# Performance work log

Hardware: AMD Instinct MI355X
Metric: run time of the kernel (lower is better)

The kernel has to match this reference:

```python
import jax, jax.numpy as jnp
import numpy as np

B, T, DIM = 1, 1024, 1024
H = 8
QLR, KVLR = 768, 512
DNOPE, DROPE, DV = 128, 64, 128
DK = DNOPE + DROPE  # 192
EPS = 1e-5


def _rms(x, w):
    return x * jax.lax.rsqrt(jnp.mean(x * x, axis=-1, keepdims=True) + EPS) * w


def _l2norm(x):
    return x * jax.lax.rsqrt(jnp.sum(x * x, axis=-1, keepdims=True) + 1e-6)


def setup_inputs() -> dict:
    key = jax.random.key(0)
    ks = jax.random.split(key, 12)
    std = 0.02
    rnd = lambda k, shape: (jax.random.normal(k, shape, dtype=jnp.float32) * std)
    return {
        'x': jax.random.normal(ks[0], (B, T, DIM), dtype=jnp.float32),
        'cos': jax.random.normal(ks[1], (T, DROPE), dtype=jnp.float32),
        'sin': jax.random.normal(ks[2], (T, DROPE), dtype=jnp.float32),
        'wq_a': rnd(ks[3], (DIM, QLR)),
        'q_norm_w': jnp.ones((QLR,), dtype=jnp.float32),
        'wq_b': rnd(ks[4], (QLR, H * DK)),
        'wkv_a': rnd(ks[5], (DIM, KVLR + DROPE)),
        'kv_norm_w': jnp.ones((KVLR,), dtype=jnp.float32),
        'wkv_b': rnd(ks[6], (KVLR, H * (DNOPE + DV))),
        'wg_w': rnd(ks[7], (DIM, H * DK)),
        'wg_b': jnp.zeros((H * DK,), dtype=jnp.float32),
        'wb': rnd(ks[8], (DIM, H)),
        'wo': rnd(ks[9], (H * DV, DIM)),
    }


def _kda(q, k, v, g, beta):
    # q,k: [B,T,H,DK]; v: [B,T,H,DV]; g: [B,T,H,DK] (log-decay); beta: [B,T,H]
    q = _l2norm(q) * (DK ** -0.5)
    k = _l2norm(k)
    # time-major for scan
    qs = jnp.moveaxis(q, 1, 0)
    ks_ = jnp.moveaxis(k, 1, 0)
    vs = jnp.moveaxis(v, 1, 0)
    gs = jnp.moveaxis(g, 1, 0)
    bs = jnp.moveaxis(beta, 1, 0)

    def step(S, inp):
        q_t, k_t, v_t, g_t, b_t = inp  # [B,H,DK],[B,H,DK],[B,H,DV],[B,H,DK],[B,H]
        S = S * jnp.exp(g_t)[..., None]                       # per-key-dim decay
        u_t = b_t[..., None] * (v_t - jnp.einsum('bhk,bhkv->bhv', k_t, S))
        S = S + k_t[..., None] * u_t[..., None, :]            # rank-1 delta update
        o_t = jnp.einsum('bhk,bhkv->bhv', q_t, S)
        return S, o_t

    S0 = jnp.zeros((B, H, DK, DV), dtype=q.dtype)
    _, o = jax.lax.scan(step, S0, (qs, ks_, vs, gs, bs))
    return jnp.moveaxis(o, 0, 1)  # [B,T,H,DV]


def reference(x, cos, sin, wq_a, q_norm_w, wq_b, wkv_a, kv_norm_w, wkv_b, wg_w, wg_b, wb, wo):
    # cos/sin are accepted but unused, matching the original forward body.
    q = (_rms(x @ wq_a, q_norm_w) @ wq_b).reshape(B, T, H, DK)
    kv_all = x @ wkv_a
    kv_c, k_pe = kv_all[..., :KVLR], kv_all[..., KVLR:]       # [B,T,KVLR],[B,T,DROPE]
    kv = (_rms(kv_c, kv_norm_w) @ wkv_b).reshape(B, T, H, DNOPE + DV)
    k_nope, v = kv[..., :DNOPE], kv[..., DNOPE:]
    k = jnp.concatenate(
        [k_nope, jnp.broadcast_to(k_pe[:, :, None, :], (B, T, H, DROPE))], axis=-1)
    g = jax.nn.log_sigmoid(x @ wg_w + wg_b).reshape(B, T, H, DK)
    beta = jax.nn.sigmoid(x @ wb).reshape(B, T, H)
    o = _kda(q, k, v, g, beta)
    o = jnp.nan_to_num(o, nan=0.0, posinf=10000.0, neginf=-10000.0)
    return o.reshape(B, T, H * DV) @ wo
```

## Files before the change

kernel.cpp:

```cpp
#include <hip/hip_runtime.h>
#include <hip/hip_bf16.h>
#include <math.h>

#define TT 1024
#define DIM 1024
#define HH 8
#define QLR 768
#define KVLR 512
#define DNOPE 128
#define DROPE 64
#define DV 128
#define DK 192
#define HDK (HH*DK)
#define HKV (HH*(DNOPE+DV))

#define OY   0
#define OQ   3072
#define OC   6144
#define OPL  9984
#define OU   10240
#define OLAM 12288
#define PABLK 12480

typedef __attribute__((ext_vector_type(8))) short short8;
typedef __attribute__((ext_vector_type(4))) float f32x4;

__device__ __forceinline__ unsigned short f2bf_rn(float f) {
    unsigned u = __float_as_uint(f);
    unsigned lsb = (u >> 16) & 1u;
    u += 0x7fffu + lsb;
    return (unsigned short)(u >> 16);
}
__device__ __forceinline__ float bf2f(unsigned short h) {
    return __uint_as_float(((unsigned)h) << 16);
}

__global__ __launch_bounds__(256) void wconv(
    const float* __restrict__ W0, unsigned short* __restrict__ H0,
    unsigned short* __restrict__ L0, int K0, int N0, int T0,
    const float* __restrict__ W1, unsigned short* __restrict__ H1,
    unsigned short* __restrict__ L1, int K1, int N1, int T1,
    const float* __restrict__ W2, unsigned short* __restrict__ H2,
    unsigned short* __restrict__ L2, int K2, int N2, int T2)
{
    __shared__ float Ls[64][65];
    int bx = blockIdx.x;
    const float* W; unsigned short* H; unsigned short* L; int K, N;
    if (bx < T0)           { W = W0; H = H0; L = L0; K = K0; N = N0; }
    else if (bx < T0 + T1) { bx -= T0; W = W1; H = H1; L = L1; K = K1; N = N1; }
    else                   { bx -= T0 + T1; W = W2; H = H2; L = L2; K = K2; N = N2; }

    const int NT = N >> 6;
    const int kt = bx / NT, nt = bx - kt * NT;
    const int k0 = kt * 64, n0 = nt * 64;
    const int tid = threadIdx.x;
    const int r = tid >> 2, c = (tid & 3) * 16;

#pragma unroll
    for (int i = 0; i < 4; i++)
        *(float4*)&Ls[r][c + i * 4] =
            *(const float4*)&W[(size_t)(k0 + r) * N + n0 + c + i * 4];
    __syncthreads();

    const int nr = tid >> 2, kc = (tid & 3) * 16;
    unsigned short hb[16], lb[16];
#pragma unroll
    for (int j = 0; j < 16; j++) {
        float v = Ls[kc + j][nr];
        unsigned short h = f2bf_rn(v);
        hb[j] = h;
        lb[j] = f2bf_rn(v - bf2f(h));
    }
    size_t ob = (size_t)(n0 + nr) * K + k0 + kc;
    *(float4*)&H[ob]     = ((float4*)hb)[0];
    *(float4*)&H[ob + 8] = ((float4*)hb)[1];
    *(float4*)&L[ob]     = ((float4*)lb)[0];
    *(float4*)&L[ob + 8] = ((float4*)lb)[1];
}

__global__ __launch_bounds__(256) void aconv(
    const float* __restrict__ A, unsigned short* __restrict__ H,
    unsigned short* __restrict__ L)
{
    int i = (blockIdx.x * 256 + threadIdx.x) * 8;
    float4 v0 = *(const float4*)&A[i];
    float4 v1 = *(const float4*)&A[i + 4];
    float vv[8] = {v0.x, v0.y, v0.z, v0.w, v1.x, v1.y, v1.z, v1.w};
    unsigned short hb[8], lb[8];
#pragma unroll
    for (int j = 0; j < 8; j++) {
        unsigned short h = f2bf_rn(vv[j]);
        hb[j] = h;
        lb[j] = f2bf_rn(vv[j] - bf2f(h));
    }
    *(float4*)&H[i] = *(float4*)hb;
    *(float4*)&L[i] = *(float4*)lb;
}

__global__ __launch_bounds__(128) void gemm_bt(
    const unsigned short* __restrict__ Ah0, const unsigned short* __restrict__ Al0,
    const unsigned short* __restrict__ Bh0, const unsigned short* __restrict__ Bl0,
    float* __restrict__ C0, int K0, int N0, int T0,
    const unsigned short* __restrict__ Ah1, const unsigned short* __restrict__ Al1,
    const unsigned short* __restrict__ Bh1, const unsigned short* __restrict__ Bl1,
    float* __restrict__ C1, int K1, int N1, int T1,
    const unsigned short* __restrict__ Ah2, const unsigned short* __restrict__ Al2,
    const unsigned short* __restrict__ Bh2, const unsigned short* __restrict__ Bl2,
    float* __restrict__ C2, int K2, int N2, int T2)
{
    __shared__ unsigned short Ahs[64 * 40], Als[64 * 40];
    __shared__ unsigned short Bhs[64 * 40], Bls[64 * 40];

    int bx = blockIdx.x;
    const unsigned short *Ah, *Al, *Bh, *Bl; float* C; int K, N;
    if (bx < T0) {
        Ah = Ah0; Al = Al0; Bh = Bh0; Bl = Bl0; C = C0; K = K0; N = N0;
    } else if (bx < T0 + T1) {
        bx -= T0; Ah = Ah1; Al = Al1; Bh = Bh1; Bl = Bl1; C = C1; K = K1; N = N1;
    } else {
        bx -= T0 + T1; Ah = Ah2; Al = Al2; Bh = Bh2; Bl = Bl2; C = C2; K = K2; N = N2;
    }

    const int tid = threadIdx.x;
    const int w = tid >> 6, l = tid & 63;
    const int q = l >> 4, m16 = l & 15;
    const int bm = blockIdx.y * 64, bn = bx * 64;

    const int c0i = tid * 2, c1i = tid * 2 + 1;
    const int r0 = c0i >> 2, o0 = (c0i & 3) * 8;
    const int r1 = c1i >> 2, o1 = (c1i & 3) * 8;
    const unsigned short* pAh0 = Ah + (size_t)(bm + r0) * K + o0;
    const unsigned short* pAh1 = Ah + (size_t)(bm + r1) * K + o1;
    const unsigned short* pAl0 = Al + (size_t)(bm + r0) * K + o0;
    const unsigned short* pAl1 = Al + (size_t)(bm + r1) * K + o1;
    const unsigned short* pBh0 = Bh + (size_t)(bn + r0) * K + o0;
    const unsigned short* pBh1 = Bh + (size_t)(bn + r1) * K + o1;
    const unsigned short* pBl0 = Bl + (size_t)(bn + r0) * K + o0;
    const unsigned short* pBl1 = Bl + (size_t)(bn + r1) * K + o1;

    f32x4 acc[2][4];
#pragma unroll
    for (int i = 0; i < 2; i++)
#pragma unroll
        for (int j = 0; j < 4; j++)
            acc[i][j] = (f32x4){0.f, 0.f, 0.f, 0.f};

    float4 vAh0 = *(const float4*)pAh0, vAh1 = *(const float4*)pAh1;
    float4 vAl0 = *(const float4*)pAl0, vAl1 = *(const float4*)pAl1;
    float4 vBh0 = *(const float4*)pBh0, vBh1 = *(const float4*)pBh1;
    float4 vBl0 = *(const float4*)pBl0, vBl1 = *(const float4*)pBl1;

    for (int k0 = 0;; k0 += 32) {
        __syncthreads();
        *(float4*)&Ahs[r0 * 40 + o0] = vAh0; *(float4*)&Ahs[r1 * 40 + o1] = vAh1;
        *(float4*)&Als[r0 * 40 + o0] = vAl0; *(float4*)&Als[r1 * 40 + o1] = vAl1;
        *(float4*)&Bhs[r0 * 40 + o0] = vBh0; *(float4*)&Bhs[r1 * 40 + o1] = vBh1;
        *(float4*)&Bls[r0 * 40 + o0] = vBl0; *(float4*)&Bls[r1 * 40 + o1] = vBl1;
        __syncthreads();

        const bool more = (k0 + 32) < K;
        if (more) {
            const int kn = k0 + 32;
            vAh0 = *(const float4*)(pAh0 + kn); vAh1 = *(const float4*)(pAh1 + kn);
            vAl0 = *(const float4*)(pAl0 + kn); vAl1 = *(const float4*)(pAl1 + kn);
            vBh0 = *(const float4*)(pBh0 + kn); vBh1 = *(const float4*)(pBh1 + kn);
            vBl0 = *(const float4*)(pBl0 + kn); vBl1 = *(const float4*)(pBl1 + kn);
        }

        short8 fah[2], fal[2], fbh[4], fbl[4];
#pragma unroll
        for (int mt = 0; mt < 2; mt++) {
            const int row = w * 32 + mt * 16 + m16;
            fah[mt] = *(const short8*)&Ahs[row * 40 + q * 8];
            fal[mt] = *(const short8*)&Als[row * 40 + q * 8];
        }
#pragma unroll
        for (int nt = 0; nt < 4; nt++) {
            const int row = nt * 16 + m16;
            fbh[nt] = *(const short8*)&Bhs[row * 40 + q * 8];
            fbl[nt] = *(const short8*)&Bls[row * 40 + q * 8];
        }
#pragma unroll
        for (int mt = 0; mt < 2; mt++)
#pragma unroll
            for (int nt = 0; nt < 4; nt++) {
                acc[mt][nt] = __builtin_amdgcn_mfma_f32_16x16x32_bf16(
                    fah[mt], fbh[nt], acc[mt][nt], 0, 0, 0);
                acc[mt][nt] = __builtin_amdgcn_mfma_f32_16x16x32_bf16(
                    fah[mt], fbl[nt], acc[mt][nt], 0, 0, 0);
                acc[mt][nt] = __builtin_amdgcn_mfma_f32_16x16x32_bf16(
                    fal[mt], fbh[nt], acc[mt][nt], 0, 0, 0);
            }
        if (!more) break;
    }

#pragma unroll
    for (int mt = 0; mt < 2; mt++)
#pragma unroll
        for (int nt = 0; nt < 4; nt++) {
            const int mrow = bm + w * 32 + mt * 16 + q * 4;
            const int ncol = bn + nt * 16 + m16;
#pragma unroll
            for (int r = 0; r < 4; r++)
                C[(size_t)(mrow + r) * N + ncol] = acc[mt][nt][r];
        }
}

__global__ __launch_bounds__(256) void rmsnorm_bf2(
    const float* __restrict__ in0, const float* __restrict__ w0,
    unsigned short* __restrict__ oh0, unsigned short* __restrict__ ol0,
    const float* __restrict__ in1, const float* __restrict__ w1,
    unsigned short* __restrict__ oh1, unsigned short* __restrict__ ol1)
{
    int bx = blockIdx.x;
    const float* in; const float* w; unsigned short *oh, *ol;
    int t, stride, ncols; float inv_n;
    if (bx < TT) {
        t = bx; in = in0; w = w0; oh = oh0; ol = ol0;
        stride = QLR; ncols = QLR; inv_n = 1.f / QLR;
    } else {
        t = bx - TT; in = in1; w = w1; oh = oh1; ol = ol1;
        stride = KVLR + DROPE; ncols = KVLR; inv_n = 1.f / KVLR;
    }
    const int tid = threadIdx.x;
    const float* row = in + (size_t)t * stride;
    float ss = 0.f;
    for (int c = tid; c < ncols; c += 256) { float v = row[c]; ss += v * v; }
#pragma unroll
    for (int m = 1; m < 64; m <<= 1) ss += __shfl_xor(ss, m);
    __shared__ float red[4];
    if ((tid & 63) == 0) red[tid >> 6] = ss;
    __syncthreads();
    float tot = red[0] + red[1] + red[2] + red[3];
    float scale = rsqrtf(tot * inv_n + 1e-5f);
    for (int c = tid; c < ncols; c += 256) {
        float v = row[c] * scale * w[c];
        unsigned short h = f2bf_rn(v);
        oh[(size_t)t * ncols + c] = h;
        ol[(size_t)t * ncols + c] = f2bf_rn(v - bf2f(h));
    }
}

__global__ __launch_bounds__(256) void small_fused(
    const float* __restrict__ g, const float* __restrict__ bias,
    float* __restrict__ la_h,
    const float* __restrict__ x, const float* __restrict__ wb,
    float* __restrict__ betab,
    const float* __restrict__ qraw, const float* __restrict__ kvb,
    const float* __restrict__ kv_all, float* __restrict__ q_h,
    float* __restrict__ k_h)
{
    int bx = blockIdx.x;
    if (bx < 6144) {
        int i = bx * 256 + threadIdx.x;
        int t = i / HDK, col = i - t * HDK;
        int h = col / DK, d = col - h * DK;
        float z = g[i] + bias[col];
        float la = fminf(z, 0.f) - log1pf(__expf(-fabsf(z)));
        la_h[((size_t)h * TT + t) * DK + d] = la;
        return;
    }
    bx -= 6144;
    const int lane = threadIdx.x & 63, wv = threadIdx.x >> 6;
    if (bx < 2048) {
        const int p = bx * 4 + wv;
        const int t = p >> 3, h = p & 7;
        const float* xr = x + (size_t)t * DIM;
        float s = 0.f;
        for (int e = lane; e < DIM; e += 64) s += xr[e] * wb[e * HH + h];
#pragma unroll
        for (int m = 1; m < 64; m <<= 1) s += __shfl_xor(s, m);
        if (lane == 0) betab[p] = 1.f / (1.f + expf(-s));
        return;
    }
    bx -= 2048;
    {
        const int p = bx * 4 + wv;
        const int t = p >> 3, h = p & 7;

        const float* qrow = qraw + (size_t)t * HDK + h * DK;
        float q0 = qrow[lane], q1 = qrow[lane + 64], q2 = qrow[lane + 128];
        float ss = q0 * q0 + q1 * q1 + q2 * q2;
#pragma unroll
        for (int m = 1; m < 64; m <<= 1) ss += __shfl_xor(ss, m);
        float sc = rsqrtf(ss + 1e-6f) * 0.07216878364870323f;
        float* qo = q_h + ((size_t)h * TT + t) * DK;
        qo[lane] = q0 * sc; qo[lane + 64] = q1 * sc; qo[lane + 128] = q2 * sc;

        const float* knope = kvb + (size_t)t * HKV + h * (DNOPE + DV);
        float k0 = knope[lane], k1 = knope[lane + 64];
        float k2 = kv_all[(size_t)t * (KVLR + DROPE) + KVLR + lane];
        float ks = k0 * k0 + k1 * k1 + k2 * k2;
#pragma unroll
        for (int m = 1; m < 64; m <<= 1) ks += __shfl_xor(ks, m);
        float kc = rsqrtf(ks + 1e-6f);
        float* ko = k_h + ((size_t)h * TT + t) * DK;
        ko[lane] = k0 * kc; ko[lane + 64] = k1 * kc; ko[lane + 128] = k2 * kc;
    }
}

__device__ __forceinline__ float dpp_xor1(float x) {
    return __int_as_float(__builtin_amdgcn_update_dpp(
        0, __float_as_int(x), 0xB1, 0xF, 0xF, false));
}
__device__ __forceinline__ float dpp_xor2(float x) {
    return __int_as_float(__builtin_amdgcn_update_dpp(
        0, __float_as_int(x), 0x4E, 0xF, 0xF, false));
}
__device__ __forceinline__ float red16(float x) {
    x += dpp_xor1(x);
    x += dpp_xor2(x);
    x += __int_as_float(__builtin_amdgcn_update_dpp(0, __float_as_int(x), 0x141, 0xF, 0xF, false));
    x += __int_as_float(__builtin_amdgcn_update_dpp(0, __float_as_int(x), 0x140, 0xF, 0xF, false));
    return x;
}

__device__ __forceinline__ void gl_lds16(const float* g, float* l) {
    __builtin_amdgcn_global_load_lds(
        (const __attribute__((address_space(1))) void*)g,
        (__attribute__((address_space(3))) void*)l, 16, 0, 0);
}
__device__ __forceinline__ void gl_lds4(const float* g, float* l) {
    __builtin_amdgcn_global_load_lds(
        (const __attribute__((address_space(1))) void*)g,
        (__attribute__((address_space(3))) void*)l, 4, 0, 0);
}

__global__ __launch_bounds__(256) void chunk_prep(
    const float* __restrict__ k_h, const float* __restrict__ la_h,
    const float* __restrict__ q_h, const float* __restrict__ kvb,
    const float* __restrict__ betab, float* __restrict__ pa)
{
    __shared__ float Ls[16][196];
    __shared__ float Ks[16][196];
    __shared__ float Qs[16][196];
    __shared__ float Ws[16][196];
    __shared__ float Xs[16][196];
    __shared__ float Ms[16][16];
    __shared__ float bs[16];

    const int tid = threadIdx.x;
    const int n = blockIdx.x >> 3, h = blockIdx.x & 7;
    const size_t g0 = ((size_t)h * TT + n * 16) * DK;
    float* blob = pa + (size_t)blockIdx.x * PABLK;

#pragma unroll
    for (int s = 0; s < 3; s++) {
        int off = (tid * 3 + s) * 4;
        int r = off / 192, c = off - r * 192;
        *(float4*)&Ks[r][c] = *(const float4*)(k_h + g0 + off);
        *(float4*)&Ls[r][c] = *(const float4*)(la_h + g0 + off);
        *(float4*)&Qs[r][c] = *(const float4*)(q_h + g0 + off);
    }
    if (tid < 16) bs[tid] = betab[(size_t)(n * 16 + tid) * HH + h];
    __syncthreads();

    if (tid < 192) {
        float g = 0.f;
#pragma unroll
        for (int i = 0; i < 16; i++) { g += Ls[i][tid]; Ls[i][tid] = g; }
    }
    __syncthreads();

#pragma unroll
    for (int s = 0; s < 12; s++) {
        int idx = s * 256 + tid;
        int i = idx / 192, d = idx - i * 192;
        float G = Ls[i][d];
        float eg = __expf(G), en = __expf(-G);
        float kk = Ks[i][d];
        Ws[i][d] = bs[i] * kk * eg;
        Qs[i][d] *= eg;
        Ks[i][d] = kk * en;
    }
    __syncthreads();

#pragma unroll
    for (int s = 0; s < 3; s++) {
        int off = (tid * 3 + s) * 4;
        int r = off / 192, c = off - r * 192;
        *(float4*)(blob + OQ + off) = *(const float4*)&Qs[r][c];
    }
    if (tid < 192) {
        float lam = __expf(Ls[15][tid]);
        blob[OLAM + tid] = lam;
#pragma unroll
        for (int j4 = 0; j4 < 4; j4++) {
            float4 v;
            v.x = Ks[j4 * 4 + 0][tid] * lam; v.y = Ks[j4 * 4 + 1][tid] * lam;
            v.z = Ks[j4 * 4 + 2][tid] * lam; v.w = Ks[j4 * 4 + 3][tid] * lam;
            *(float4*)(blob + OC + tid * 20 + j4 * 4) = v;
        }
        blob[OC + tid * 20 + 16] = 0.f; blob[OC + tid * 20 + 17] = 0.f;
        blob[OC + tid * 20 + 18] = 0.f; blob[OC + tid * 20 + 19] = 0.f;
    }
    {
        const int i = tid >> 4, j = tid & 15;
        float m = 0.f, p = 0.f;
#pragma unroll
        for (int d4 = 0; d4 < 48; d4++) {
            float4 w  = *(const float4*)&Ws[i][d4 * 4];
            float4 ka = *(const float4*)&Ks[j][d4 * 4];
            float4 qa = *(const float4*)&Qs[i][d4 * 4];
            m += w.x * ka.x + w.y * ka.y + w.z * ka.z + w.w * ka.w;
            p += qa.x * ka.x + qa.y * ka.y + qa.z * ka.z + qa.w * ka.w;
        }
        Ms[i][j] = (j < i) ? m : 0.f;
        blob[OPL + tid] = (j <= i) ? p : 0.f;
    }
    __syncthreads();

    float y[16], uu[16];
    const bool doY = (tid < 192);
    const bool doU = (tid >= 128);
    const int dcol = tid, ccol = tid - 128;
    if (doY) {
#pragma unroll
        for (int i = 0; i < 16; i++) y[i] = Ws[i][dcol];
#pragma unroll
        for (int i = 1; i < 16; i++)
#pragma unroll
            for (int j = 0; j < i; j++)
                y[i] = fmaf(-Ms[i][j], y[j], y[i]);
    }
    if (doU) {
#pragma unroll
        for (int i = 0; i < 16; i++)
            uu[i] = bs[i] * kvb[(size_t)(n * 16 + i) * HKV + h * (DNOPE + DV) + DNOPE + ccol];
#pragma unroll
        for (int i = 1; i < 16; i++)
#pragma unroll
            for (int j = 0; j < i; j++)
                uu[i] = fmaf(-Ms[i][j], uu[j], uu[i]);
    }
    if (doY) {
#pragma unroll
        for (int i = 0; i < 16; i++) Xs[i][dcol] = y[i];
    }
    __syncthreads();
#pragma unroll
    for (int s = 0; s < 3; s++) {
        int off = (tid * 3 + s) * 4;
        int r = off / 192, c = off - r * 192;
        *(float4*)(blob + OY + off) = *(const float4*)&Xs[r][c];
    }
    __syncthreads();
    if (doU) {
#pragma unroll
        for (int i = 0; i < 16; i++) Xs[i][ccol] = uu[i];
    }
    __syncthreads();
#pragma unroll
    for (int s = 0; s < 2; s++) {
        int off = (tid * 2 + s) * 4;
        int r = off / 128, c = off - r * 128;
        *(float4*)(blob + OU + off) = *(const float4*)&Xs[r][c];
    }
}

__global__ __launch_bounds__(256) void kda_chunk(
    const float* __restrict__ pa, unsigned short* __restrict__ obh,
    unsigned short* __restrict__ obl)
{
    __shared__ float Cb[3][3840];
    __shared__ float Pb[3][256];
    __shared__ float ubs[3][64];
    __shared__ float lbs[3][192];
    __shared__ float Ss[784];
    __shared__ float us[80];

    const int tid = threadIdx.x;
    const int w = tid >> 6, lane = tid & 63;
    const int h = blockIdx.x >> 5, cg = blockIdx.x & 31;
    const int c0 = cg * 4;

    const int dg  = tid & 15;
    const int ccg = (tid >> 4) & 1;
    const int tig = tid >> 5;
    const int dbase = dg * 12;

    auto stage = [&](int buf, int n) {
        const float* blob = pa + (size_t)(n * 8 + h) * PABLK;
        if (w == 0) {
#pragma unroll
            for (int s = 0; s < 8; s++)
                gl_lds16(blob + OC + s * 256 + lane * 4, &Cb[buf][s * 256]);
        } else if (w == 1) {
#pragma unroll
            for (int s = 8; s < 15; s++)
                gl_lds16(blob + OC + s * 256 + lane * 4, &Cb[buf][s * 256]);
        } else if (w == 2) {
            gl_lds16(blob + OPL + lane * 4, &Pb[buf][0]);
            gl_lds4(blob + OU + (lane >> 2) * 128 + c0 + (lane & 3), &ubs[buf][0]);
            if (lane < 48)
                gl_lds16(blob + OLAM + lane * 4, &lbs[buf][0]);
        }
    };

    auto ldYQ = [&](int n, float4 (&Y)[2][3], float4 (&Q)[2][3]) {
        const float* blob = pa + (size_t)(n * 8 + h) * PABLK;
#pragma unroll
        for (int i = 0; i < 2; i++) {
            const float* py = blob + OY + (tig * 2 + i) * 192 + dbase;
            const float* pq = blob + OQ + (tig * 2 + i) * 192 + dbase;
#pragma unroll
            for (int s = 0; s < 3; s++) {
                Y[i][s] = *(const float4*)(py + s * 4);
                Q[i][s] = *(const float4*)(pq + s * 4);
            }
        }
    };

    for (int idx = tid; idx < 784; idx += 256) Ss[idx] = 0.f;
    stage(0, 0);
    stage(1, 1);

    float4 YA[2][3], QA[2][3], YB[2][3], QB[2][3];
    ldYQ(0, YA, QA);

    const int c2 = tid & 3, dseg = tid >> 2;

    auto body = [&](int n, int bf, float4 (&Yc)[2][3], float4 (&Qc)[2][3],
                    float4 (&Yn)[2][3], float4 (&Qn)[2][3]) {
        __syncthreads();

        if (n + 2 < TT / 16) {
            int b2 = bf + 2; if (b2 >= 3) b2 -= 3;
            stage(b2, n + 2);
        }
        {
            int np = n + 1; if (np > TT / 16 - 1) np = TT / 16 - 1;
            ldYQ(np, Yn, Qn);
        }

        float4 sv[2][3];
#pragma unroll
        for (int j = 0; j < 2; j++)
#pragma unroll
            for (int s = 0; s < 3; s++)
                sv[j][s] = *(const float4*)&Ss[(ccg * 2 + j) * 196 + dbase + s * 4];

        float py[2][2] = {{0.f, 0.f}, {0.f, 0.f}};
        float pq[2][2] = {{0.f, 0.f}, {0.f, 0.f}};
#pragma unroll
        for (int i = 0; i < 2; i++)
#pragma unroll
            for (int s = 0; s < 3; s++) {
                float4 yv = Yc[i][s];
                float4 qv = Qc[i][s];
#pragma unroll
                for (int j = 0; j < 2; j++) {
                    float4 s4 = sv[j][s];
                    py[i][j] = fmaf(yv.x, s4.x, py[i][j]);
                    py[i][j] = fmaf(yv.y, s4.y, py[i][j]);
                    py[i][j] = fmaf(yv.z, s4.z, py[i][j]);
                    py[i][j] = fmaf(yv.w, s4.w, py[i][j]);
                    pq[i][j] = fmaf(qv.x, s4.x, pq[i][j]);
                    pq[i][j] = fmaf(qv.y, s4.y, pq[i][j]);
                    pq[i][j] = fmaf(qv.z, s4.z, pq[i][j]);
                    pq[i][j] = fmaf(qv.w, s4.w, pq[i][j]);
                }
            }
        float zy[2][2], zq[2][2];
#pragma unroll
        for (int i = 0; i < 2; i++)
#pragma unroll
            for (int j = 0; j < 2; j++) {
                zy[i][j] = red16(py[i][j]);
                zq[i][j] = red16(pq[i][j]);
            }

        float uv[2][2];
#pragma unroll
        for (int i = 0; i < 2; i++)
#pragma unroll
            for (int j = 0; j < 2; j++)
                uv[i][j] = ubs[bf][(tig * 2 + i) * 4 + (ccg * 2 + j)] - zy[i][j];
        {
            const int m = dg >> 2;
            if ((dg & 3) == 0) {
                const int ii = m >> 1, jj = m & 1;
                float val = (m == 0) ? uv[0][0] : (m == 1) ? uv[0][1]
                          : (m == 2) ? uv[1][0] : uv[1][1];
                us[(ccg * 2 + jj) * 20 + (tig * 2 + ii)] = val;
            }
        }
        __syncthreads();

        {
            const int m = dg >> 2, qtr = dg & 3;
            const int ii = m >> 1, jj = m & 1;
            const int ti = tig * 2 + ii, cc = ccg * 2 + jj;
            float acc = 0.f;
            for (int j = qtr; j <= ti; j += 4)
                acc = fmaf(Pb[bf][ti * 16 + j], us[cc * 20 + j], acc);
            acc += dpp_xor1(acc);
            acc += dpp_xor2(acc);
            if (qtr == 0) {
                float zqv = (m == 0) ? zq[0][0] : (m == 1) ? zq[0][1]
                          : (m == 2) ? zq[1][0] : zq[1][1];
                float ov = zqv + acc;
                if (isnan(ov)) ov = 0.f;
                else if (isinf(ov)) ov = ov > 0.f ? 1e4f : -1e4f;
                size_t oi = (size_t)(n * 16 + ti) * (HH * DV) + h * DV + c0 + cc;
                unsigned short hb = f2bf_rn(ov);
                obh[oi] = hb;
                obl[oi] = f2bf_rn(ov - bf2f(hb));
            }
        }

        const float4* up = (const float4*)&us[c2 * 20];
        float4 u0 = up[0], u1 = up[1], u2v = up[2], u3 = up[3];
#pragma unroll
        for (int s = 0; s < 3; s++) {
            int d = dseg * 3 + s;
            float svv = Ss[c2 * 196 + d];
            float a2 = lbs[bf][d] * svv;
            const float4* C4 = (const float4*)&Cb[bf][d * 20];
            float4 k0 = C4[0], k1 = C4[1], k2 = C4[2], k3 = C4[3];
            a2 = fmaf(k0.x, u0.x,  a2); a2 = fmaf(k0.y, u0.y,  a2);
            a2 = fmaf(k0.z, u0.z,  a2); a2 = fmaf(k0.w, u0.w,  a2);
            a2 = fmaf(k1.x, u1.x,  a2); a2 = fmaf(k1.y, u1.y,  a2);
            a2 = fmaf(k1.z, u1.z,  a2); a2 = fmaf(k1.w, u1.w,  a2);
            a2 = fmaf(k2.x, u2v.x, a2); a2 = fmaf(k2.y, u2v.y, a2);
            a2 = fmaf(k2.z, u2v.z, a2); a2 = fmaf(k2.w, u2v.w, a2);
            a2 = fmaf(k3.x, u3.x,  a2); a2 = fmaf(k3.y, u3.y,  a2);
            a2 = fmaf(k3.z, u3.z,  a2); a2 = fmaf(k3.w, u3.w,  a2);
            Ss[c2 * 196 + d] = a2;
        }
    };

    int buf = 0;
    for (int n = 0; n < TT / 16; n += 2) {
        body(n, buf, YA, QA, YB, QB);
        int b1 = buf + 1; if (b1 >= 3) b1 -= 3;
        body(n + 1, b1, YB, QB, YA, QA);
        buf += 2; if (buf >= 3) buf -= 3;
    }
}

extern "C" void kernel_launch(void* const* d_in, const int* in_sizes, int n_in,
                              void* d_out, int out_size, void* d_ws, size_t ws_size,
                              hipStream_t stream)
{
    const float* x         = (const float*)d_in[0];
    const float* wq_a      = (const float*)d_in[3];
    const float* q_norm_w  = (const float*)d_in[4];
    const float* wq_b      = (const float*)d_in[5];
    const float* wkv_a     = (const float*)d_in[6];
    const float* kv_norm_w = (const float*)d_in[7];
    const float* wkv_b     = (const float*)d_in[8];
    const float* wg_w      = (const float*)d_in[9];
    const float* wg_b      = (const float*)d_in[10];
    const float* wb        = (const float*)d_in[11];
    const float* wo        = (const float*)d_in[12];
    float* out = (float*)d_out;

    float* ws = (float*)d_ws;
    float* xq     = ws;
    float* kv_all = xq     + TT * QLR;
    float* agraw  = kv_all + TT * (KVLR + DROPE);
    float* qnraw  = agraw  + TT * HDK;
    float* kvb    = qnraw  + TT * HDK;
    float* la_h   = kvb    + TT * HKV;
    float* q_h    = la_h   + TT * HDK;
    float* k_h    = q_h    + TT * HDK;
    float* betab  = k_h    + TT * HDK;
    float* pa     = betab  + TT * HH;
    float* tail   = pa     + 512 * PABLK;

    unsigned short* wo_h  = (unsigned short*)tail;
    unsigned short* wo_l  = wo_h  + 1048576;
    unsigned short* xh    = wo_l  + 1048576;
    unsigned short* xl    = xh    + 1048576;
    unsigned short* xqh   = xl    + 1048576;
    unsigned short* xql   = xqh   + 786432;
    unsigned short* kvnh  = xql   + 786432;
    unsigned short* kvnl  = kvnh  + 524288;

    unsigned short* wqa_h  = (unsigned short*)pa;
    unsigned short* wqa_l  = wqa_h  + 786432;
    unsigned short* wkva_h = wqa_l  + 786432;
    unsigned short* wkva_l = wkva_h + 589824;
    unsigned short* wgw_h  = wkva_l + 589824;
    unsigned short* wgw_l  = wgw_h  + 1572864;
    unsigned short* wqb_h  = wgw_l  + 1572864;
    unsigned short* wqb_l  = wqb_h  + 1179648;
    unsigned short* wkvb_h = wqb_l  + 1179648;
    unsigned short* wkvb_l = wkvb_h + 1048576;

    unsigned short* obh = (unsigned short*)agraw;
    unsigned short* obl = obh + 1048576;

    dim3 blk(256);

    wconv<<<dim3(192 + 144 + 384), blk, 0, stream>>>(
        wq_a, wqa_h, wqa_l, DIM, QLR, 192,
        wkv_a, wkva_h, wkva_l, DIM, KVLR + DROPE, 144,
        wg_w, wgw_h, wgw_l, DIM, HDK, 384);
    wconv<<<dim3(288 + 256 + 256), blk, 0, stream>>>(
        wq_b, wqb_h, wqb_l, QLR, HDK, 288,
        wkv_b, wkvb_h, wkvb_l, KVLR, HKV, 256,
        wo, wo_h, wo_l, DIM, DIM, 256);

    aconv<<<dim3(TT * DIM / (256 * 8)), blk, 0, stream>>>(x, xh, xl);

    gemm_bt<<<dim3(12 + 9 + 24, 16), dim3(128), 0, stream>>>(
        xh, xl, wqa_h, wqa_l, xq, DIM, QLR, 12,
        xh, xl, wkva_h, wkva_l, kv_all, DIM, KVLR + DROPE, 9,
        xh, xl, wgw_h, wgw_l, agraw, DIM, HDK, 24);

    rmsnorm_bf2<<<dim3(2 * TT), blk, 0, stream>>>(
        xq, q_norm_w, xqh, xql,
        kv_all, kv_norm_w, kvnh, kvnl);

    gemm_bt<<<dim3(24 + 32, 16), dim3(128), 0, stream>>>(
        xqh, xql, wqb_h, wqb_l, qnraw, QLR, HDK, 24,
        kvnh, kvnl, wkvb_h, wkvb_l, kvb, KVLR, HKV, 32,
        xh, xl, wqa_h, wqa_l, xq, DIM, QLR, 0);

    small_fused<<<dim3(6144 + 2048 + 2048), blk, 0, stream>>>(
        agraw, wg_b, la_h,
        x, wb, betab,
        qnraw, kvb, kv_all, q_h, k_h);

    chunk_prep<<<512, blk, 0, stream>>>(k_h, la_h, q_h, kvb, betab, pa);
    kda_chunk<<<256, blk, 0, stream>>>(pa, obh, obl);

    gemm_bt<<<dim3(16, 16), dim3(128), 0, stream>>>(
        obh, obl, wo_h, wo_l, out, DIM, DIM, 16,
        xh, xl, wqa_h, wqa_l, xq, DIM, QLR, 0,
        xh, xl, wqa_h, wqa_l, xq, DIM, QLR, 0);
}
```

Measured before the change: 320.8 us.

## Split KDA chunk recurrence into two value columns per block, doubling grid

Each kda_chunk block now owns 2 value columns of a head instead of 4, so the launch grows from 256 to 512 blocks. Per-block state and LDS shrink, and the intra-chunk triangular reduction uses an 8-lane DPP reduction. The aim is to shorten the serial per-chunk critical path and fill more CUs on the sequential scan. The cost is that every block still stages the full C/P/lambda chunk data, so redundant global loads double, and half the threads sit idle in the state update.

```diff
diff --git a/kernel.cpp b/kernel.cpp
--- a/kernel.cpp
+++ b/kernel.cpp
@@ -307,11 +307,21 @@
     return __int_as_float(__builtin_amdgcn_update_dpp(
         0, __float_as_int(x), 0x4E, 0xF, 0xF, false));
 }
+__device__ __forceinline__ float dpp_hm(float x) {
+    return __int_as_float(__builtin_amdgcn_update_dpp(
+        0, __float_as_int(x), 0x141, 0xF, 0xF, false));
+}
 __device__ __forceinline__ float red16(float x) {
     x += dpp_xor1(x);
     x += dpp_xor2(x);
-    x += __int_as_float(__builtin_amdgcn_update_dpp(0, __float_as_int(x), 0x141, 0xF, 0xF, false));
+    x += dpp_hm(x);
     x += __int_as_float(__builtin_amdgcn_update_dpp(0, __float_as_int(x), 0x140, 0xF, 0xF, false));
+    return x;
+}
+__device__ __forceinline__ float red8(float x) {
+    x += dpp_xor1(x);
+    x += dpp_xor2(x);
+    x += dpp_hm(x);
     return x;
 }
 
@@ -464,18 +474,18 @@
 {
     __shared__ float Cb[3][3840];
     __shared__ float Pb[3][256];
-    __shared__ float ubs[3][64];
+    __shared__ float ubs[3][32];
     __shared__ float lbs[3][192];
-    __shared__ float Ss[784];
-    __shared__ float us[80];
+    __shared__ float Ss[392];
+    __shared__ float us[40];
 
     const int tid = threadIdx.x;
     const int w = tid >> 6, lane = tid & 63;
-    const int h = blockIdx.x >> 5, cg = blockIdx.x & 31;
-    const int c0 = cg * 4;
+    const int h = blockIdx.x >> 6, cg = blockIdx.x & 63;
+    const int c0 = cg * 2;
 
     const int dg  = tid & 15;
-    const int ccg = (tid >> 4) & 1;
+    const int cc  = (tid >> 4) & 1;
     const int tig = tid >> 5;
     const int dbase = dg * 12;
 
@@ -491,7 +501,8 @@
                 gl_lds16(blob + OC + s * 256 + lane * 4, &Cb[buf][s * 256]);
         } else if (w == 2) {
             gl_lds16(blob + OPL + lane * 4, &Pb[buf][0]);
-            gl_lds4(blob + OU + (lane >> 2) * 128 + c0 + (lane & 3), &ubs[buf][0]);
+            if (lane < 32)
+                gl_lds4(blob + OU + (lane >> 1) * 128 + c0 + (lane & 1), &ubs[buf][0]);
             if (lane < 48)
                 gl_lds16(blob + OLAM + lane * 4, &lbs[buf][0]);
         }
@@ -511,14 +522,14 @@
         }
     };
 
-    for (int idx = tid; idx < 784; idx += 256) Ss[idx] = 0.f;
+    for (int idx = tid; idx < 392; idx += 256) Ss[idx] = 0.f;
     stage(0, 0);
     stage(1, 1);
 
     float4 YA[2][3], QA[2][3], YB[2][3], QB[2][3];
     ldYQ(0, YA, QA);
 
-    const int c2 = tid & 3, dseg = tid >> 2;
+    const int c2 = tid & 1, dseg = tid >> 1;
 
     auto body = [&](int n, int bf, float4 (&Yc)[2][3], float4 (&Qc)[2][3],
                     float4 (&Yn)[2][3], float4 (&Qn)[2][3]) {
@@ -533,73 +544,56 @@
             ldYQ(np, Yn, Qn);
         }
 
-        float4 sv[2][3];
-#pragma unroll
-        for (int j = 0; j < 2; j++)
-#pragma unroll
-            for (int s = 0; s < 3; s++)
-                sv[j][s] = *(const float4*)&Ss[(ccg * 2 + j) * 196 + dbase + s * 4];
-
-        float py[2][2] = {{0.f, 0.f}, {0.f, 0.f}};
-        float pq[2][2] = {{0.f, 0.f}, {0.f, 0.f}};
+        float4 sv[3];
+#pragma unroll
+        for (int s = 0; s < 3; s++)
+            sv[s] = *(const float4*)&Ss[cc * 196 + dbase + s * 4];
+
+        float py[2] = {0.f, 0.f};
+        float pq[2] = {0.f, 0.f};
 #pragma unroll
         for (int i = 0; i < 2; i++)
 #pragma unroll
             for (int s = 0; s < 3; s++) {
                 float4 yv = Yc[i][s];
                 float4 qv = Qc[i][s];
-#pragma unroll
-                for (int j = 0; j < 2; j++) {
-                    float4 s4 = sv[j][s];
-                    py[i][j] = fmaf(yv.x, s4.x, py[i][j]);
-                    py[i][j] = fmaf(yv.y, s4.y, py[i][j]);
-                    py[i][j] = fmaf(yv.z, s4.z, py[i][j]);
-                    py[i][j] = fmaf(yv.w, s4.w, py[i][j]);
-                    pq[i][j] = fmaf(qv.x, s4.x, pq[i][j]);
-                    pq[i][j] = fmaf(qv.y, s4.y, pq[i][j]);
-                    pq[i][j] = fmaf(qv.z, s4.z, pq[i][j]);
-                    pq[i][j] = fmaf(qv.w, s4.w, pq[i][j]);
-                }
+                float4 s4 = sv[s];
+                py[i] = fmaf(yv.x, s4.x, py[i]);
+                py[i] = fmaf(yv.y, s4.y, py[i]);
+                py[i] = fmaf(yv.z, s4.z, py[i]);
+                py[i] = fmaf(yv.w, s4.w, py[i]);
+                pq[i] = fmaf(qv.x, s4.x, pq[i]);
+                pq[i] = fmaf(qv.y, s4.y, pq[i]);
+                pq[i] = fmaf(qv.z, s4.z, pq[i]);
+                pq[i] = fmaf(qv.w, s4.w, pq[i]);
             }
-        float zy[2][2], zq[2][2];
+        float zy[2], zq[2];
+#pragma unroll
+        for (int i = 0; i < 2; i++) {
+            zy[i] = red16(py[i]);
+            zq[i] = red16(pq[i]);
+        }
+
+        float uv[2];
 #pragma unroll
         for (int i = 0; i < 2; i++)
-#pragma unroll
-            for (int j = 0; j < 2; j++) {
-                zy[i][j] = red16(py[i][j]);
-                zq[i][j] = red16(pq[i][j]);
-            }
-
-        float uv[2][2];
-#pragma unroll
-        for (int i = 0; i < 2; i++)
-#pragma unroll
-            for (int j = 0; j < 2; j++)
-                uv[i][j] = ubs[bf][(tig * 2 + i) * 4 + (ccg * 2 + j)] - zy[i][j];
+            uv[i] = ubs[bf][(tig * 2 + i) * 2 + cc] - zy[i];
+        if ((dg & 7) == 0) {
+            const int ii = dg >> 3;
+            us[cc * 20 + tig * 2 + ii] = (ii == 0) ? uv[0] : uv[1];
+        }
+        __syncthreads();
+
         {
-            const int m = dg >> 2;
-            if ((dg & 3) == 0) {
-                const int ii = m >> 1, jj = m & 1;
-                float val = (m == 0) ? uv[0][0] : (m == 1) ? uv[0][1]
-                          : (m == 2) ? uv[1][0] : uv[1][1];
-                us[(ccg * 2 + jj) * 20 + (tig * 2 + ii)] = val;
-            }
-        }
-        __syncthreads();
-
-        {
-            const int m = dg >> 2, qtr = dg & 3;
-            const int ii = m >> 1, jj = m & 1;
-            const int ti = tig * 2 + ii, cc = ccg * 2 + jj;
+            const int ii = dg >> 3, qtr = dg & 7;
+            const int ti = tig * 2 + ii;
             float acc = 0.f;
-            for (int j = qtr; j <= ti; j += 4)
-                acc = fmaf(Pb[bf][ti * 16 + j], us[cc * 20 + j], acc);
-            acc += dpp_xor1(acc);
-            acc += dpp_xor2(acc);
+#pragma unroll
+            for (int j = qtr; j <= 15; j += 8)
+                if (j <= ti) acc = fmaf(Pb[bf][ti * 16 + j], us[cc * 20 + j], acc);
+            acc = red8(acc);
             if (qtr == 0) {
-                float zqv = (m == 0) ? zq[0][0] : (m == 1) ? zq[0][1]
-                          : (m == 2) ? zq[1][0] : zq[1][1];
-                float ov = zqv + acc;
+                float ov = zq[ii] + acc;
                 if (isnan(ov)) ov = 0.f;
                 else if (isinf(ov)) ov = ov > 0.f ? 1e4f : -1e4f;
                 size_t oi = (size_t)(n * 16 + ti) * (HH * DV) + h * DV + c0 + cc;
@@ -609,24 +603,26 @@
             }
         }
 
-        const float4* up = (const float4*)&us[c2 * 20];
-        float4 u0 = up[0], u1 = up[1], u2v = up[2], u3 = up[3];
-#pragma unroll
-        for (int s = 0; s < 3; s++) {
-            int d = dseg * 3 + s;
-            float svv = Ss[c2 * 196 + d];
-            float a2 = lbs[bf][d] * svv;
-            const float4* C4 = (const float4*)&Cb[bf][d * 20];
-            float4 k0 = C4[0], k1 = C4[1], k2 = C4[2], k3 = C4[3];
-            a2 = fmaf(k0.x, u0.x,  a2); a2 = fmaf(k0.y, u0.y,  a2);
-            a2 = fmaf(k0.z, u0.z,  a2); a2 = fmaf(k0.w, u0.w,  a2);
-            a2 = fmaf(k1.x, u1.x,  a2); a2 = fmaf(k1.y, u1.y,  a2);
-            a2 = fmaf(k1.z, u1.z,  a2); a2 = fmaf(k1.w, u1.w,  a2);
-            a2 = fmaf(k2.x, u2v.x, a2); a2 = fmaf(k2.y, u2v.y, a2);
-            a2 = fmaf(k2.z, u2v.z, a2); a2 = fmaf(k2.w, u2v.w, a2);
-            a2 = fmaf(k3.x, u3.x,  a2); a2 = fmaf(k3.y, u3.y,  a2);
-            a2 = fmaf(k3.z, u3.z,  a2); a2 = fmaf(k3.w, u3.w,  a2);
-            Ss[c2 * 196 + d] = a2;
+        if (tid < 128) {
+            const float4* up = (const float4*)&us[c2 * 20];
+            float4 u0 = up[0], u1 = up[1], u2v = up[2], u3 = up[3];
+#pragma unroll
+            for (int s = 0; s < 3; s++) {
+                int d = dseg * 3 + s;
+                float svv = Ss[c2 * 196 + d];
+                float a2 = lbs[bf][d] * svv;
+                const float4* C4 = (const float4*)&Cb[bf][d * 20];
+                float4 k0 = C4[0], k1 = C4[1], k2 = C4[2], k3 = C4[3];
+                a2 = fmaf(k0.x, u0.x,  a2); a2 = fmaf(k0.y, u0.y,  a2);
+                a2 = fmaf(k0.z, u0.z,  a2); a2 = fmaf(k0.w, u0.w,  a2);
+                a2 = fmaf(k1.x, u1.x,  a2); a2 = fmaf(k1.y, u1.y,  a2);
+                a2 = fmaf(k1.z, u1.z,  a2); a2 = fmaf(k1.w, u1.w,  a2);
+                a2 = fmaf(k2.x, u2v.x, a2); a2 = fmaf(k2.y, u2v.y, a2);
+                a2 = fmaf(k2.z, u2v.z, a2); a2 = fmaf(k2.w, u2v.w, a2);
+                a2 = fmaf(k3.x, u3.x,  a2); a2 = fmaf(k3.y, u3.y,  a2);
+                a2 = fmaf(k3.z, u3.z,  a2); a2 = fmaf(k3.w, u3.w,  a2);
+                Ss[c2 * 196 + d] = a2;
+            }
         }
     };
 
@@ -725,7 +721,7 @@
         qnraw, kvb, kv_all, q_h, k_h);
 
     chunk_prep<<<512, blk, 0, stream>>>(k_h, la_h, q_h, kvb, betab, pa);
-    kda_chunk<<<256, blk, 0, stream>>>(pa, obh, obl);
+    kda_chunk<<<512, blk, 0, stream>>>(pa, obh, obl);
 
     gemm_bt<<<dim3(16, 16), dim3(128), 0, stream>>>(
         obh, obl, wo_h, wo_l, out, DIM, DIM, 16,
```

Result: no change. 316.7 us (-1.3%).
